# Optimization experiments

Hardware: AMD Instinct MI355X
Metric: run time of the kernel (lower is better)

The kernel has to match this reference:

```python
import math
import jax, jax.numpy as jnp
import numpy as np

N_EMBD = 1024
N_HEAD = 16
HEAD_DIM = N_EMBD // N_HEAD
B, T = 4, 2048
LN_EPS = 1e-5


def setup_inputs() -> dict:
    key = jax.random.key(0)
    ks = jax.random.split(key, 20)
    s = 0.02
    d = {
        'x': jax.random.normal(ks[0], (B, T, N_EMBD), jnp.float32),
        'Wq': jax.random.normal(ks[1], (N_EMBD, N_EMBD), jnp.float32) * s,
        'bq': jnp.zeros((N_EMBD,), jnp.float32),
        'Wk': jax.random.normal(ks[2], (N_EMBD, N_EMBD), jnp.float32) * s,
        'bk': jnp.zeros((N_EMBD,), jnp.float32),
        'Wv': jax.random.normal(ks[3], (N_EMBD, N_EMBD), jnp.float32) * s,
        'bv': jnp.zeros((N_EMBD,), jnp.float32),
        'Wo': jax.random.normal(ks[4], (N_EMBD, N_EMBD), jnp.float32) * s,
        'bo': jnp.zeros((N_EMBD,), jnp.float32),
        'ln1_g': jnp.ones((N_EMBD,), jnp.float32),
        'ln1_b': jnp.zeros((N_EMBD,), jnp.float32),
        'ln2_g': jnp.ones((N_EMBD,), jnp.float32),
        'ln2_b': jnp.zeros((N_EMBD,), jnp.float32),
        'W_fc': jax.random.normal(ks[5], (N_EMBD, 4 * N_EMBD), jnp.float32) * s,
        'b_fc': jnp.zeros((4 * N_EMBD,), jnp.float32),
        'W_proj': jax.random.normal(ks[6], (4 * N_EMBD, N_EMBD), jnp.float32) * s,
        'b_proj': jnp.zeros((N_EMBD,), jnp.float32),
    }
    return d


def _layernorm(x, g, b):
    mu = jnp.mean(x, axis=-1, keepdims=True)
    var = jnp.var(x, axis=-1, keepdims=True)
    return (x - mu) * jax.lax.rsqrt(var + LN_EPS) * g + b


def _new_gelu(x):
    c = math.sqrt(2.0 / math.pi)
    return 0.5 * x * (1.0 + jnp.tanh(c * (x + 0.044715 * x ** 3)))


def _attn(x, Wq, bq, Wk, bk, Wv, bv, Wo, bo):
    Bq, Tq, C = x.shape
    def heads(y):  # (B,T,C) -> (B,H,T,D)
        return y.reshape(Bq, Tq, N_HEAD, HEAD_DIM).transpose(0, 2, 1, 3)
    q = heads(x @ Wq + bq)
    k = heads(x @ Wk + bk)
    v = heads(x @ Wv + bv)
    scores = jnp.einsum('bhqd,bhkd->bhqk', q, k) / math.sqrt(HEAD_DIM)
    causal = jnp.tril(jnp.ones((Tq, Tq), bool))
    scores = jnp.where(causal, scores, -jnp.inf)
    w = jax.nn.softmax(scores, axis=-1)
    av = jnp.einsum('bhqk,bhkd->bhqd', w, v)
    av = av.transpose(0, 2, 1, 3).reshape(Bq, Tq, C)
    return av @ Wo + bo


def reference(x, Wq, bq, Wk, bk, Wv, bv, Wo, bo, ln1_g, ln1_b, ln2_g, ln2_b, W_fc, b_fc, W_proj, b_proj):
    x = x + _attn(_layernorm(x, ln1_g, ln1_b), Wq, bq, Wk, bk, Wv, bv, Wo, bo)
    h = _layernorm(x, ln2_g, ln2_b)
    x = x + (_new_gelu(h @ W_fc + b_fc) @ W_proj + b_proj)
    return x
```

## Files before the change

### kernel.cpp

```cpp
#include <hip/hip_runtime.h>

typedef __attribute__((ext_vector_type(8))) short short8;
typedef __attribute__((ext_vector_type(4))) short short4v;
typedef __attribute__((ext_vector_type(4))) float floatx4;
typedef unsigned short u16;

#define MFMA16(a,b,c) __builtin_amdgcn_mfma_f32_16x16x32_bf16(a,b,c,0,0,0)

typedef const __attribute__((address_space(1))) void* gas1;
typedef __attribute__((address_space(3))) void* las3;
static __device__ __forceinline__ void glds16(const void* g, void* l){
  __builtin_amdgcn_global_load_lds((gas1)g, (las3)l, 16, 0, 0);
}

static __device__ __forceinline__ u16 f2b(float f){
  union { float f; unsigned int u; } c; c.f = f;
  unsigned int u = c.u;
  u += 0x7fffu + ((u >> 16) & 1u);
  return (u16)(u >> 16);
}

__global__ __launch_bounds__(256) void transpose_cvt(
    const float* __restrict__ W, u16* __restrict__ Wt, int K, int N){
  __shared__ float tile[32][33];
  const int tx = threadIdx.x & 31;
  const int ty = threadIdx.x >> 5;
  const int nx = blockIdx.x * 32, kx = blockIdx.y * 32;
  #pragma unroll
  for (int i = ty; i < 32; i += 8)
    tile[i][tx] = W[(size_t)(kx + i) * N + nx + tx];
  __syncthreads();
  #pragma unroll
  for (int i = ty; i < 32; i += 8)
    Wt[(size_t)(nx + i) * K + kx + tx] = f2b(tile[tx][i]);
}

__global__ __launch_bounds__(256) void ln_kernel(
    const float* __restrict__ x, const float* __restrict__ g,
    const float* __restrict__ b, u16* __restrict__ out){
  const int row = blockIdx.x, tid = threadIdx.x;
  const float4 v = reinterpret_cast<const float4*>(x + (size_t)row * 1024)[tid];
  float s  = v.x + v.y + v.z + v.w;
  float s2 = v.x*v.x + v.y*v.y + v.z*v.z + v.w*v.w;
  #pragma unroll
  for (int off = 1; off < 64; off <<= 1){
    s  += __shfl_xor(s,  off);
    s2 += __shfl_xor(s2, off);
  }
  __shared__ float red[8];
  const int wave = tid >> 6, lane = tid & 63;
  if (lane == 0){ red[wave] = s; red[4 + wave] = s2; }
  __syncthreads();
  s  = red[0] + red[1] + red[2] + red[3];
  s2 = red[4] + red[5] + red[6] + red[7];
  const float mu  = s * (1.f/1024.f);
  const float var = s2 * (1.f/1024.f) - mu * mu;
  const float rs  = rsqrtf(var + 1e-5f);
  const float4 gg = reinterpret_cast<const float4*>(g)[tid];
  const float4 bb = reinterpret_cast<const float4*>(b)[tid];
  ushort4 o;
  o.x = f2b((v.x - mu) * rs * gg.x + bb.x);
  o.y = f2b((v.y - mu) * rs * gg.y + bb.y);
  o.z = f2b((v.z - mu) * rs * gg.z + bb.z);
  o.w = f2b((v.w - mu) * rs * gg.w + bb.w);
  reinterpret_cast<ushort4*>(out + (size_t)row * 1024)[tid] = o;
}

__global__ __launch_bounds__(256) void bias_concat(
    const float* __restrict__ bq, const float* __restrict__ bk,
    const float* __restrict__ bv, float* __restrict__ o){
  const int i = blockIdx.x * 256 + threadIdx.x;
  if (i < 1024) o[i] = bq[i];
  else if (i < 2048) o[i] = bk[i - 1024];
  else if (i < 3072) o[i] = bv[i - 2048];
}

template<bool GELU, bool RES, bool OUTBF, bool QKVMODE>
__global__ __launch_bounds__(256) void gemm128(
    const u16* __restrict__ A, const u16* __restrict__ Bt,
    const float* __restrict__ bias, const float* __restrict__ bias2,
    const float* __restrict__ bias3,
    const float* __restrict__ res,
    float* __restrict__ outF, u16* __restrict__ outB,
    u16* __restrict__ vtb,
    int M, int N, int K)
{
  __shared__ __attribute__((aligned(16))) u16 sA[2][128 * 32];
  __shared__ __attribute__((aligned(16))) u16 sB[2][128 * 32];
  const int tid  = threadIdx.x;
  const int wave = tid >> 6, lane = tid & 63, quad = lane >> 4, l16 = lane & 15;
  const int m0 = blockIdx.x * 128, n0 = blockIdx.y * 128;
  const int wm = (wave >> 1) * 64, wn = (wave & 1) * 64;

  const int scol = ((lane & 3) ^ ((lane >> 3) & 3)) * 8;
  const size_t aoff = (size_t)(m0 + wave*32 + (lane >> 2)) * K + scol;
  const size_t boff = (size_t)(n0 + wave*32 + (lane >> 2)) * K + scol;
  const size_t half = (size_t)16 * K;
  u16* alp = sA[0] + wave * 1024;
  u16* blp = sB[0] + wave * 1024;
  const int qx = (quad ^ ((l16 >> 1) & 3)) * 8;

  floatx4 acc[4][4];
  #pragma unroll
  for (int i = 0; i < 4; i++)
    #pragma unroll
    for (int nt = 0; nt < 4; nt++) acc[i][nt] = floatx4{0.f,0.f,0.f,0.f};

  for (int k0 = 0; k0 < K; k0 += 64){
    #pragma unroll
    for (int c = 0; c < 2; c++){
      glds16(A  + aoff + k0 + c*32,        alp + c*4096);
      glds16(A  + aoff + k0 + c*32 + half, alp + c*4096 + 512);
      glds16(Bt + boff + k0 + c*32,        blp + c*4096);
      glds16(Bt + boff + k0 + c*32 + half, blp + c*4096 + 512);
    }
    __syncthreads();
    #pragma unroll
    for (int c = 0; c < 2; c++){
      short8 af[4], bf[4];
      #pragma unroll
      for (int i = 0; i < 4; i++)
        af[i] = *reinterpret_cast<const short8*>(&sA[c][(wm + i*16 + l16)*32 + qx]);
      #pragma unroll
      for (int nt = 0; nt < 4; nt++)
        bf[nt] = *reinterpret_cast<const short8*>(&sB[c][(wn + nt*16 + l16)*32 + qx]);
      #pragma unroll
      for (int i = 0; i < 4; i++)
        #pragma unroll
        for (int nt = 0; nt < 4; nt++)
          acc[i][nt] = MFMA16(af[i], bf[nt], acc[i][nt]);
    }
    __syncthreads();
  }

  if (QKVMODE && n0 >= 2048){
    #pragma unroll
    for (int nt = 0; nt < 4; nt++){
      const int hd = n0 + wn + nt*16 + l16 - 2048;
      const float bi = bias3[hd];
      u16* vcol = vtb + (size_t)(hd >> 6) * 131072 + (size_t)(hd & 63) * 2048;
      #pragma unroll
      for (int i = 0; i < 4; i++){
        const int t0 = m0 + wm + i*16 + quad*4;
        const int bb = t0 >> 11, tt = t0 & 2047;
        short4v pk;
        #pragma unroll
        for (int r = 0; r < 4; r++) pk[r] = (short)f2b(acc[i][nt][r] + bi);
        *reinterpret_cast<short4v*>(vcol + (size_t)bb * 2097152 + tt) = pk;
      }
    }
    return;
  }

  #pragma unroll
  for (int nt = 0; nt < 4; nt++){
    const int col = n0 + wn + nt*16 + l16;
    float bi;
    if (QKVMODE) bi = (col < 1024) ? bias[col] : bias2[col-1024];
    else         bi = bias[col];
    #pragma unroll
    for (int i = 0; i < 4; i++){
      #pragma unroll
      for (int r = 0; r < 4; r++){
        const int row = m0 + wm + i*16 + quad*4 + r;
        float val = acc[i][nt][r] + bi;
        if (GELU){
          const float t = 0.7978845608028654f * (val + 0.044715f * val * val * val);
          val = val / (1.f + __expf(-2.f * t));
        }
        if (RES) val += res[(size_t)row * N + col];
        if (OUTBF) outB[(size_t)row * N + col] = f2b(val);
        else       outF[(size_t)row * N + col] = val;
      }
    }
  }
}

__global__ __launch_bounds__(256) void attn_kernel(
    const u16* __restrict__ qkv, const u16* __restrict__ vtb,
    u16* __restrict__ O)
{
  constexpr int T = 2048, LDQ = 3072, LDP = 72;
  __shared__ __attribute__((aligned(16))) u16 sK[2][2][64*32];
  __shared__ __attribute__((aligned(16))) u16 sV[2][2][64*32];
  __shared__ __attribute__((aligned(16))) u16 sP[4][16*LDP];

  const int tid = threadIdx.x, wave = tid >> 6, lane = tid & 63;
  const int quad = lane >> 4, l16 = lane & 15;

  const int lin = blockIdx.y * 16 + blockIdx.x;
  const int j = lin & 15;
  const int bh = lin >> 4;
  const int kk4 = bh >> 4;
  const int jj = (j + ((kk4 & 2) << 2)) & 15;
  const int qt = (kk4 & 1) ? (15 - jj) : jj;
  const int q0 = qt * 128;
  const int b = bh >> 4, h = bh & 15;

  const u16* Qp = qkv + (size_t)b * T * LDQ + h * 64;
  const u16* Kp = Qp + 1024;
  const u16* Vt = vtb + (size_t)bh * 64 * T;

  const int qx = (quad ^ ((l16 >> 1) & 3)) * 8;

  int qg[2]; qg[0] = q0 + wave*16 + l16; qg[1] = qg[0] + 64;
  short8 qf[2][2];
  #pragma unroll
  for (int g = 0; g < 2; g++){
    qf[g][0] = *reinterpret_cast<const short8*>(&Qp[(size_t)qg[g]*LDQ + quad*8]);
    qf[g][1] = *reinterpret_cast<const short8*>(&Qp[(size_t)qg[g]*LDQ + 32 + quad*8]);
  }

  float m_i[2] = {-INFINITY, -INFINITY}, l_i[2] = {0.f, 0.f};
  floatx4 o_acc[2][4];
  #pragma unroll
  for (int g = 0; g < 2; g++)
    #pragma unroll
    for (int nt = 0; nt < 4; nt++) o_acc[g][nt] = floatx4{0.f,0.f,0.f,0.f};

  const int srow = wave*16 + (lane >> 2);
  const int scol = ((lane & 3) ^ ((lane >> 3) & 3)) * 8;
  const int asrc = (lane & 48) | (quad * 4);

  const int kend = q0 + 128;

  {
    glds16(Kp + (size_t)srow*LDQ + scol,      sK[0][0] + wave*512);
    glds16(Kp + (size_t)srow*LDQ + 32 + scol, sK[0][1] + wave*512);
    glds16(Vt + (size_t)srow*T + scol,        sV[0][0] + wave*512);
    glds16(Vt + (size_t)srow*T + 32 + scol,   sV[0][1] + wave*512);
  }

  int buf = 0;
  for (int k0 = 0; k0 < kend; k0 += 64, buf ^= 1){
    __syncthreads();
    if (k0 + 64 < kend){
      const int kn = k0 + 64;
      glds16(Kp + (size_t)(kn + srow)*LDQ + scol,      sK[buf^1][0] + wave*512);
      glds16(Kp + (size_t)(kn + srow)*LDQ + 32 + scol, sK[buf^1][1] + wave*512);
      glds16(Vt + (size_t)srow*T + kn + scol,          sV[buf^1][0] + wave*512);
      glds16(Vt + (size_t)srow*T + kn + 32 + scol,     sV[buf^1][1] + wave*512);
    }

    #pragma unroll
    for (int g = 0; g < 2; g++){
      if (g == 0 && k0 > q0) continue;

      float s[4][4];
      #pragma unroll
      for (int sub = 0; sub < 4; sub++){
        floatx4 sa = floatx4{0.f,0.f,0.f,0.f};
        const short8 kf0 = *reinterpret_cast<const short8*>(&sK[buf][0][(sub*16 + l16)*32 + qx]);
        const short8 kf1 = *reinterpret_cast<const short8*>(&sK[buf][1][(sub*16 + l16)*32 + qx]);
        sa = MFMA16(kf0, qf[g][0], sa);
        sa = MFMA16(kf1, qf[g][1], sa);
        #pragma unroll
        for (int r = 0; r < 4; r++) s[sub][r] = sa[r];
      }
      if (k0 == q0 + g*64){
        #pragma unroll
        for (int sub = 0; sub < 4; sub++)
          #pragma unroll
          for (int r = 0; r < 4; r++){
            const int kidx = k0 + sub*16 + quad*4 + r;
            if (kidx > qg[g]) s[sub][r] = -1e30f;
          }
      }

      float mx = s[0][0];
      #pragma unroll
      for (int sub = 0; sub < 4; sub++)
        #pragma unroll
        for (int r = 0; r < 4; r++) mx = fmaxf(mx, s[sub][r]);
      mx = fmaxf(mx, __shfl_xor(mx, 16));
      mx = fmaxf(mx, __shfl_xor(mx, 32));
      const float mnew  = fmaxf(m_i[g], mx);
      const float alpha = __expf(0.125f * (m_i[g] - mnew));
      float p[4][4], rowsum = 0.f;
      #pragma unroll
      for (int sub = 0; sub < 4; sub++)
        #pragma unroll
        for (int r = 0; r < 4; r++){
          p[sub][r] = __expf(0.125f * (s[sub][r] - mnew));
          rowsum += p[sub][r];
        }
      rowsum += __shfl_xor(rowsum, 16);
      rowsum += __shfl_xor(rowsum, 32);
      l_i[g] = l_i[g] * alpha + rowsum;
      m_i[g] = mnew;

      float arow[4];
      #pragma unroll
      for (int r = 0; r < 4; r++) arow[r] = __shfl(alpha, asrc + r);
      #pragma unroll
      for (int nt = 0; nt < 4; nt++)
        #pragma unroll
        for (int r = 0; r < 4; r++) o_acc[g][nt][r] *= arow[r];

      #pragma unroll
      for (int sub = 0; sub < 4; sub++){
        short4v pk;
        pk[0] = (short)f2b(p[sub][0]); pk[1] = (short)f2b(p[sub][1]);
        pk[2] = (short)f2b(p[sub][2]); pk[3] = (short)f2b(p[sub][3]);
        *reinterpret_cast<short4v*>(&sP[wave][l16*LDP + sub*16 + quad*4]) = pk;
      }
      const short8 pf0 = *reinterpret_cast<const short8*>(&sP[wave][l16*LDP + quad*8]);
      const short8 pf1 = *reinterpret_cast<const short8*>(&sP[wave][l16*LDP + 32 + quad*8]);
      #pragma unroll
      for (int nt = 0; nt < 4; nt++){
        const short8 vf0 = *reinterpret_cast<const short8*>(&sV[buf][0][(nt*16 + l16)*32 + qx]);
        const short8 vf1 = *reinterpret_cast<const short8*>(&sV[buf][1][(nt*16 + l16)*32 + qx]);
        o_acc[g][nt] = MFMA16(pf0, vf0, o_acc[g][nt]);
        o_acc[g][nt] = MFMA16(pf1, vf1, o_acc[g][nt]);
      }
    }
  }

  #pragma unroll
  for (int g = 0; g < 2; g++){
    float lrow[4];
    #pragma unroll
    for (int r = 0; r < 4; r++) lrow[r] = __shfl(l_i[g], asrc + r);
    #pragma unroll
    for (int nt = 0; nt < 4; nt++){
      #pragma unroll
      for (int r = 0; r < 4; r++){
        const int row = q0 + g*64 + wave*16 + quad*4 + r;
        O[(size_t)(b*T + row)*1024 + h*64 + nt*16 + l16] = f2b(o_acc[g][nt][r] / lrow[r]);
      }
    }
  }
}

extern "C" void kernel_launch(void* const* d_in, const int* in_sizes, int n_in,
                              void* d_out, int out_size, void* d_ws, size_t ws_size,
                              hipStream_t stream){
  const float* x      = (const float*)d_in[0];
  const float* Wq     = (const float*)d_in[1];
  const float* bq     = (const float*)d_in[2];
  const float* Wk     = (const float*)d_in[3];
  const float* bk     = (const float*)d_in[4];
  const float* Wv     = (const float*)d_in[5];
  const float* bv     = (const float*)d_in[6];
  const float* Wo     = (const float*)d_in[7];
  const float* bo     = (const float*)d_in[8];
  const float* ln1_g  = (const float*)d_in[9];
  const float* ln1_b  = (const float*)d_in[10];
  const float* ln2_g  = (const float*)d_in[11];
  const float* ln2_b  = (const float*)d_in[12];
  const float* W_fc   = (const float*)d_in[13];
  const float* b_fc   = (const float*)d_in[14];
  const float* W_proj = (const float*)d_in[15];
  const float* b_proj = (const float*)d_in[16];
  float* out = (float*)d_out;
  char* ws = (char*)d_ws;
  const size_t MB = 1024 * 1024;

  u16* bufA  = (u16*)(ws);
  u16* qkvb  = (u16*)(ws + 16*MB);
  u16* vtb   = (u16*)(ws + 64*MB);
  u16* fcb   = (u16*)(ws + 16*MB);
  float* x2  = out;
  u16* Wqkvt = (u16*)(ws + 80*MB);
  u16* Wot   = (u16*)(ws + 86*MB);
  u16* Wfct  = (u16*)(ws + 88*MB);
  u16* Wpjt  = (u16*)(ws + 96*MB);
  float* bqkv= (float*)(ws + 104*MB);

  dim3 tb(256);
  transpose_cvt<<<dim3(32, 32),  tb, 0, stream>>>(Wq,     Wqkvt,             1024, 1024);
  transpose_cvt<<<dim3(32, 32),  tb, 0, stream>>>(Wk,     Wqkvt + 1024*1024, 1024, 1024);
  transpose_cvt<<<dim3(32, 32),  tb, 0, stream>>>(Wv,     Wqkvt + 2048*1024, 1024, 1024);
  transpose_cvt<<<dim3(32, 32),  tb, 0, stream>>>(Wo,     Wot,               1024, 1024);
  transpose_cvt<<<dim3(128, 32), tb, 0, stream>>>(W_fc,   Wfct,              1024, 4096);
  transpose_cvt<<<dim3(32, 128), tb, 0, stream>>>(W_proj, Wpjt,              4096, 1024);
  bias_concat<<<dim3(12), tb, 0, stream>>>(bq, bk, bv, bqkv);

  ln_kernel<<<8192, tb, 0, stream>>>(x, ln1_g, ln1_b, bufA);

  gemm128<false,false,true,true><<<dim3(64,24), tb, 0, stream>>>(
      bufA, Wqkvt, bqkv, bqkv+1024, bqkv+2048, nullptr, nullptr, qkvb, vtb, 8192, 3072, 1024);

  attn_kernel<<<dim3(16, 64), tb, 0, stream>>>(qkvb, vtb, bufA);

  gemm128<false,true,false,false><<<dim3(64,8), tb, 0, stream>>>(
      bufA, Wot, bo, nullptr, nullptr, x, x2, nullptr, nullptr, 8192, 1024, 1024);

  ln_kernel<<<8192, tb, 0, stream>>>(x2, ln2_g, ln2_b, bufA);

  gemm128<true,false,true,false><<<dim3(64,32), tb, 0, stream>>>(
      bufA, Wfct, b_fc, nullptr, nullptr, nullptr, nullptr, fcb, nullptr, 8192, 4096, 1024);

  gemm128<false,true,false,false><<<dim3(64,8), tb, 0, stream>>>(
      fcb, Wpjt, b_proj, nullptr, nullptr, x2, out, nullptr, nullptr, 8192, 1024, 4096);
}
```

Baseline: 559.1 us.

## Double-buffer GEMM K-loop and permute B rows for vectorized epilogue stores

The GEMM main loop now prefetches the next 32-wide K slice into the alternate LDS buffer while computing on the current one, replacing the load-all-then-compute 64-wide step that had two barriers per iteration. The B-tile rows are loaded in permuted order so each lane owns four consecutive output columns. This lets the epilogue use vector bias loads, vector residual reads and vector stores (4 floats or 4 bf16) instead of scalar per-element writes. The risk is that the smaller K step doubles the number of barriers per unit of K, and correctness depends on the row permutation lining up with the column indexing used in the epilogue.

```diff
diff --git a/kernel.cpp b/kernel.cpp
--- a/kernel.cpp
+++ b/kernel.cpp
@@ -78,8 +78,7 @@
 template<bool GELU, bool RES, bool OUTBF, bool QKVMODE>
 __global__ __launch_bounds__(256) void gemm128(
     const u16* __restrict__ A, const u16* __restrict__ Bt,
-    const float* __restrict__ bias, const float* __restrict__ bias2,
-    const float* __restrict__ bias3,
+    const float* __restrict__ bias,
     const float* __restrict__ res,
     float* __restrict__ outF, u16* __restrict__ outB,
     u16* __restrict__ vtb,
@@ -93,9 +92,11 @@
   const int wm = (wave >> 1) * 64, wn = (wave & 1) * 64;
 
   const int scol = ((lane & 3) ^ ((lane >> 3) & 3)) * 8;
-  const size_t aoff = (size_t)(m0 + wave*32 + (lane >> 2)) * K + scol;
-  const size_t boff = (size_t)(n0 + wave*32 + (lane >> 2)) * K + scol;
-  const size_t half = (size_t)16 * K;
+  const size_t aoff  = (size_t)(m0 + wave*32 + (lane >> 2)) * K + scol;
+  const size_t aoff2 = aoff + (size_t)16 * K;
+  const int brow = n0 + (wave >> 1)*64 + 4*(lane >> 2) + (wave & 1)*2;
+  const size_t boff  = (size_t)brow * K + scol;
+  const size_t boff2 = boff + (size_t)K;
   u16* alp = sA[0] + wave * 1024;
   u16* blp = sB[0] + wave * 1024;
   const int qx = (quad ^ ((l16 >> 1) & 3)) * 8;
@@ -106,38 +107,45 @@
     #pragma unroll
     for (int nt = 0; nt < 4; nt++) acc[i][nt] = floatx4{0.f,0.f,0.f,0.f};
 
-  for (int k0 = 0; k0 < K; k0 += 64){
-    #pragma unroll
-    for (int c = 0; c < 2; c++){
-      glds16(A  + aoff + k0 + c*32,        alp + c*4096);
-      glds16(A  + aoff + k0 + c*32 + half, alp + c*4096 + 512);
-      glds16(Bt + boff + k0 + c*32,        blp + c*4096);
-      glds16(Bt + boff + k0 + c*32 + half, blp + c*4096 + 512);
-    }
+  glds16(A  + aoff,  alp);
+  glds16(A  + aoff2, alp + 512);
+  glds16(Bt + boff,  blp);
+  glds16(Bt + boff2, blp + 512);
+
+  int buf = 0;
+  for (int k0 = 0; k0 < K; k0 += 32, buf ^= 1){
     __syncthreads();
-    #pragma unroll
-    for (int c = 0; c < 2; c++){
-      short8 af[4], bf[4];
-      #pragma unroll
-      for (int i = 0; i < 4; i++)
-        af[i] = *reinterpret_cast<const short8*>(&sA[c][(wm + i*16 + l16)*32 + qx]);
+    if (k0 + 32 < K){
+      const int kn = k0 + 32;
+      const int bo = (buf ^ 1) * 4096;
+      glds16(A  + aoff  + kn, alp + bo);
+      glds16(A  + aoff2 + kn, alp + bo + 512);
+      glds16(Bt + boff  + kn, blp + bo);
+      glds16(Bt + boff2 + kn, blp + bo + 512);
+    }
+    const u16* sa = sA[buf];
+    const u16* sb = sB[buf];
+    short8 af[4], bf[4];
+    #pragma unroll
+    for (int i = 0; i < 4; i++)
+      af[i] = *reinterpret_cast<const short8*>(&sa[(wm + i*16 + l16)*32 + qx]);
+    #pragma unroll
+    for (int nt = 0; nt < 4; nt++)
+      bf[nt] = *reinterpret_cast<const short8*>(&sb[(wn + nt*16 + l16)*32 + qx]);
+    #pragma unroll
+    for (int i = 0; i < 4; i++)
       #pragma unroll
       for (int nt = 0; nt < 4; nt++)
-        bf[nt] = *reinterpret_cast<const short8*>(&sB[c][(wn + nt*16 + l16)*32 + qx]);
-      #pragma unroll
-      for (int i = 0; i < 4; i++)
-        #pragma unroll
-        for (int nt = 0; nt < 4; nt++)
-          acc[i][nt] = MFMA16(af[i], bf[nt], acc[i][nt]);
-    }
-    __syncthreads();
-  }
+        acc[i][nt] = MFMA16(af[i], bf[nt], acc[i][nt]);
+  }
+
+  const int col0 = n0 + wn + 4*l16;
+  const floatx4 bi = *reinterpret_cast<const floatx4*>(&bias[col0]);
 
   if (QKVMODE && n0 >= 2048){
     #pragma unroll
     for (int nt = 0; nt < 4; nt++){
-      const int hd = n0 + wn + nt*16 + l16 - 2048;
-      const float bi = bias3[hd];
+      const int hd = col0 + nt - 2048;
       u16* vcol = vtb + (size_t)(hd >> 6) * 131072 + (size_t)(hd & 63) * 2048;
       #pragma unroll
       for (int i = 0; i < 4; i++){
@@ -145,7 +153,7 @@
         const int bb = t0 >> 11, tt = t0 & 2047;
         short4v pk;
         #pragma unroll
-        for (int r = 0; r < 4; r++) pk[r] = (short)f2b(acc[i][nt][r] + bi);
+        for (int r = 0; r < 4; r++) pk[r] = (short)f2b(acc[i][nt][r] + bi[nt]);
         *reinterpret_cast<short4v*>(vcol + (size_t)bb * 2097152 + tt) = pk;
       }
     }
@@ -153,24 +161,32 @@
   }
 
   #pragma unroll
-  for (int nt = 0; nt < 4; nt++){
-    const int col = n0 + wn + nt*16 + l16;
-    float bi;
-    if (QKVMODE) bi = (col < 1024) ? bias[col] : bias2[col-1024];
-    else         bi = bias[col];
-    #pragma unroll
-    for (int i = 0; i < 4; i++){
-      #pragma unroll
-      for (int r = 0; r < 4; r++){
-        const int row = m0 + wm + i*16 + quad*4 + r;
-        float val = acc[i][nt][r] + bi;
-        if (GELU){
-          const float t = 0.7978845608028654f * (val + 0.044715f * val * val * val);
-          val = val / (1.f + __expf(-2.f * t));
+  for (int i = 0; i < 4; i++){
+    #pragma unroll
+    for (int r = 0; r < 4; r++){
+      const int row = m0 + wm + i*16 + quad*4 + r;
+      if (OUTBF){
+        short4v o;
+        #pragma unroll
+        for (int nt = 0; nt < 4; nt++){
+          float val = acc[i][nt][r] + bi[nt];
+          if (GELU){
+            const float t = 0.7978845608028654f * (val + 0.044715f * val * val * val);
+            val = val / (1.f + __expf(-2.f * t));
+          }
+          o[nt] = (short)f2b(val);
         }
-        if (RES) val += res[(size_t)row * N + col];
-        if (OUTBF) outB[(size_t)row * N + col] = f2b(val);
-        else       outF[(size_t)row * N + col] = val;
+        *reinterpret_cast<short4v*>(&outB[(size_t)row * N + col0]) = o;
+      } else {
+        floatx4 v;
+        #pragma unroll
+        for (int nt = 0; nt < 4; nt++) v[nt] = acc[i][nt][r] + bi[nt];
+        if (RES){
+          const floatx4 rr = *reinterpret_cast<const floatx4*>(&res[(size_t)row * N + col0]);
+          #pragma unroll
+          for (int nt = 0; nt < 4; nt++) v[nt] += rr[nt];
+        }
+        *reinterpret_cast<floatx4*>(&outF[(size_t)row * N + col0]) = v;
       }
     }
   }
@@ -379,18 +395,18 @@
   ln_kernel<<<8192, tb, 0, stream>>>(x, ln1_g, ln1_b, bufA);
 
   gemm128<false,false,true,true><<<dim3(64,24), tb, 0, stream>>>(
-      bufA, Wqkvt, bqkv, bqkv+1024, bqkv+2048, nullptr, nullptr, qkvb, vtb, 8192, 3072, 1024);
+      bufA, Wqkvt, bqkv, nullptr, nullptr, qkvb, vtb, 8192, 3072, 1024);
 
   attn_kernel<<<dim3(16, 64), tb, 0, stream>>>(qkvb, vtb, bufA);
 
   gemm128<false,true,false,false><<<dim3(64,8), tb, 0, stream>>>(
-      bufA, Wot, bo, nullptr, nullptr, x, x2, nullptr, nullptr, 8192, 1024, 1024);
+      bufA, Wot, bo, x, x2, nullptr, nullptr, 8192, 1024, 1024);
 
   ln_kernel<<<8192, tb, 0, stream>>>(x2, ln2_g, ln2_b, bufA);
 
   gemm128<true,false,true,false><<<dim3(64,32), tb, 0, stream>>>(
-      bufA, Wfct, b_fc, nullptr, nullptr, nullptr, nullptr, fcb, nullptr, 8192, 4096, 1024);
+      bufA, Wfct, b_fc, nullptr, nullptr, fcb, nullptr, 8192, 4096, 1024);
 
   gemm128<false,true,false,false><<<dim3(64,8), tb, 0, stream>>>(
-      fcb, Wpjt, b_proj, nullptr, nullptr, x2, out, nullptr, nullptr, 8192, 1024, 4096);
-}
+      fcb, Wpjt, b_proj, x2, out, nullptr, nullptr, 8192, 1024, 4096);
+}
```

Result: faster. 544.8 us (-2.5%).
